# Kernel tuning notes

Measured on AMD Instinct MI355X. Metric: run time of the kernel, lower is better.

The kernel has to match this reference:

```python
import jax, jax.numpy as jnp
import numpy as np

B, D, H = 32, 512, 1024


def setup_inputs() -> dict:
    key = jax.random.key(0)
    ks = jax.random.split(key, 9)
    x = jax.random.normal(ks[0], (B, D), dtype=jnp.float32)
    h0 = 0.1 * jax.random.normal(ks[1], (B, H), dtype=jnp.float32)
    c0 = 0.1 * jax.random.normal(ks[2], (B, H), dtype=jnp.float32)
    # Hebbian trace lives in [-1, 1] (clipped each step)
    Hebb0 = jax.random.uniform(ks[3], (B, H, H), dtype=jnp.float32, minval=-0.5, maxval=0.5)
    weight_h = jax.random.normal(ks[4], (H, 4 * H), dtype=jnp.float32) / np.sqrt(H)
    weight_x = jax.random.normal(ks[5], (D, 4 * H), dtype=jnp.float32) / np.sqrt(D)
    # bias init: zeros, forget-gate slice set to 1 (T_max=None path)
    bias = jnp.zeros((4 * H,), dtype=jnp.float32).at[:H].set(1.0)
    # alpha init is constant 0.01; add tiny noise for non-degenerate testing
    alpha = 0.01 + 0.001 * jax.random.normal(ks[6], (H, H), dtype=jnp.float32)
    eta = jnp.array([0.01], dtype=jnp.float32)
    return {"x": x, "h0": h0, "c0": c0, "Hebb0": Hebb0,
            "weight_h": weight_h, "weight_x": weight_x, "bias": bias,
            "alpha": alpha, "eta": eta}


def reference(x, h0, c0, Hebb0, weight_h, weight_x, bias, alpha, eta):
    Hs = h0.shape[1]
    # gates = h0 @ (weight_h + cat[0,0,0, alpha*Hebb]) + x @ weight_x + bias
    # The plastic term only affects the last (cell-gate) chunk; compute it
    # without materializing the (B,H,4H) dynamic weight tensor.
    gates = h0 @ weight_h + x @ weight_x + bias[None, :]
    plastic = jnp.einsum('bi,ih,bih->bh', h0, alpha, Hebb0)  # (B, H)
    f_g, i_g, o_g, g_g = jnp.split(gates, 4, axis=1)
    g_g = g_g + plastic  # cell gate gets the fast-weight contribution
    tanh_g = jnp.tanh(g_g)
    c1 = jax.nn.sigmoid(f_g) * c0 + jax.nn.sigmoid(i_g) * tanh_g
    h1 = jax.nn.sigmoid(o_g) * jnp.tanh(c1)
    # Hebbian outer-product update with clip (neuromodulation=None path)
    Hebb1 = jnp.clip(Hebb0 + eta[0] * jnp.einsum('bh,bi->bhi', h0, tanh_g), -1.0, 1.0)
    return h1, c1, Hebb1
```

## Files before the change

kernel.cpp:

```cpp
#include <hip/hip_runtime.h>
#include <math.h>

#define B 32
#define D 512
#define H 1024
#define G4 4096
#define PCH 32
#define GCH 24

__global__ __launch_bounds__(256) void k_plastic(
    const float* __restrict__ h0, const float* __restrict__ alpha,
    const float* __restrict__ hebb, float* __restrict__ pp) {
  int blk = blockIdx.x;
  int b = blk >> 5;
  int c = blk & (PCH - 1);
  int h4 = threadIdx.x * 4;
  int i0 = c * (H / PCH);
  const float* hb = hebb + (size_t)b * H * H;
  float4 acc = make_float4(0.f, 0.f, 0.f, 0.f);
#pragma unroll 8
  for (int i = i0; i < i0 + (H / PCH); ++i) {
    float hv = h0[b * H + i];
    float4 a = *(const float4*)(alpha + (size_t)i * H + h4);
    float4 e = *(const float4*)(hb + (size_t)i * H + h4);
    acc.x += hv * a.x * e.x;
    acc.y += hv * a.y * e.y;
    acc.z += hv * a.z * e.z;
    acc.w += hv * a.w * e.w;
  }
  *(float4*)(pp + ((size_t)c * B + b) * H + h4) = acc;
}

__global__ __launch_bounds__(256) void k_gates(
    const float* __restrict__ h0, const float* __restrict__ x,
    const float* __restrict__ wh, const float* __restrict__ wx,
    float* __restrict__ gp) {
  int j = blockIdx.x * 256 + threadIdx.x;
  int c = blockIdx.y;
  float acc[B];
#pragma unroll
  for (int b = 0; b < B; ++b) acc[b] = 0.f;
  if (c < 16) {
    int i0 = c * 64;
#pragma unroll 8
    for (int i = i0; i < i0 + 64; ++i) {
      float w = wh[(size_t)i * G4 + j];
#pragma unroll
      for (int b = 0; b < B; ++b) acc[b] += h0[b * H + i] * w;
    }
  } else {
    int i0 = (c - 16) * 64;
#pragma unroll 8
    for (int i = i0; i < i0 + 64; ++i) {
      float w = wx[(size_t)i * G4 + j];
#pragma unroll
      for (int b = 0; b < B; ++b) acc[b] += x[b * D + i] * w;
    }
  }
#pragma unroll
  for (int b = 0; b < B; ++b) gp[((size_t)c * B + b) * G4 + j] = acc[b];
}

__global__ __launch_bounds__(256) void k_combine(
    const float* __restrict__ gp, const float* __restrict__ pp,
    const float* __restrict__ bias, const float* __restrict__ c0,
    float* __restrict__ out, float* __restrict__ tg_out) {
  int t = blockIdx.x * 256 + threadIdx.x;
  int b = t >> 10;
  int h = t & (H - 1);
  float sf = bias[h], si = bias[H + h], so = bias[2 * H + h], sg = bias[3 * H + h];
#pragma unroll
  for (int c = 0; c < GCH; ++c) {
    const float* g = gp + ((size_t)c * B + b) * G4;
    sf += g[h];
    si += g[H + h];
    so += g[2 * H + h];
    sg += g[3 * H + h];
  }
#pragma unroll
  for (int c = 0; c < PCH; ++c) sg += pp[((size_t)c * B + b) * H + h];
  float fg = 1.f / (1.f + expf(-sf));
  float ig = 1.f / (1.f + expf(-si));
  float og = 1.f / (1.f + expf(-so));
  float tgv = tanhf(sg);
  float c1 = fg * c0[t] + ig * tgv;
  float h1 = og * tanhf(c1);
  out[t] = h1;
  out[B * H + t] = c1;
  tg_out[t] = tgv;
}

__global__ __launch_bounds__(256) void k_hebb(
    const float* __restrict__ hebb, const float* __restrict__ h0,
    const float* __restrict__ tg, const float* __restrict__ eta,
    float* __restrict__ out) {
  int blk = blockIdx.x;
  int b = blk >> 7;
  int hg = blk & 127;
  int t4 = threadIdx.x * 4;
  float4 tv = *(const float4*)(tg + b * H + t4);
  float e = eta[0];
  size_t base = ((size_t)b * H + (size_t)hg * 8) * H + t4;
  const float* src = hebb + base;
  float* dst = out + base;
#pragma unroll
  for (int r = 0; r < 8; ++r) {
    float s = e * h0[b * H + hg * 8 + r];
    float4 v = *(const float4*)(src + (size_t)r * H);
    float4 rr;
    rr.x = fminf(fmaxf(v.x + s * tv.x, -1.f), 1.f);
    rr.y = fminf(fmaxf(v.y + s * tv.y, -1.f), 1.f);
    rr.z = fminf(fmaxf(v.z + s * tv.z, -1.f), 1.f);
    rr.w = fminf(fmaxf(v.w + s * tv.w, -1.f), 1.f);
    *(float4*)(dst + (size_t)r * H) = rr;
  }
}

extern "C" void kernel_launch(void* const* d_in, const int* in_sizes, int n_in,
                              void* d_out, int out_size, void* d_ws, size_t ws_size,
                              hipStream_t stream) {
  const float* x     = (const float*)d_in[0];
  const float* h0    = (const float*)d_in[1];
  const float* c0    = (const float*)d_in[2];
  const float* hebb  = (const float*)d_in[3];
  const float* wh    = (const float*)d_in[4];
  const float* wx    = (const float*)d_in[5];
  const float* bias  = (const float*)d_in[6];
  const float* alpha = (const float*)d_in[7];
  const float* eta   = (const float*)d_in[8];
  float* out = (float*)d_out;
  float* ws  = (float*)d_ws;

  float* pp = ws;
  float* gp = pp + (size_t)PCH * B * H;
  float* tg = gp + (size_t)GCH * B * G4;

  k_plastic<<<B * PCH, 256, 0, stream>>>(h0, alpha, hebb, pp);
  k_gates<<<dim3(16, GCH), 256, 0, stream>>>(h0, x, wh, wx, gp);
  k_combine<<<(B * H) / 256, 256, 0, stream>>>(gp, pp, bias, c0, out, tg);
  k_hebb<<<B * 128, 256, 0, stream>>>(hebb, h0, tg, eta, out + 2 * B * H);
}
```

Measured before the change: 326.0 us.

## Merge plastic and gate partial kernels into one heterogeneous launch

Folds the plastic-term reduction and the gate GEMV partials into a single kernel, with block index selecting the role, so both run concurrently instead of back-to-back. Split-K chunk counts are halved (fewer partials for the combine step to sum), and each gate block now covers 128 rows in two 16-batch halves to cut register pressure. The trade-off is longer per-block work and possible load imbalance between the two block types.

```diff
diff --git a/kernel.cpp b/kernel.cpp
--- a/kernel.cpp
+++ b/kernel.cpp
@@ -5,60 +5,61 @@
 #define D 512
 #define H 1024
 #define G4 4096
-#define PCH 32
-#define GCH 24
+#define PCH 16
+#define GCH 12
+#define NGATE (16 * GCH)
+#define NPLAST (B * PCH)
 
-__global__ __launch_bounds__(256) void k_plastic(
-    const float* __restrict__ h0, const float* __restrict__ alpha,
-    const float* __restrict__ hebb, float* __restrict__ pp) {
-  int blk = blockIdx.x;
-  int b = blk >> 5;
-  int c = blk & (PCH - 1);
-  int h4 = threadIdx.x * 4;
-  int i0 = c * (H / PCH);
-  const float* hb = hebb + (size_t)b * H * H;
-  float4 acc = make_float4(0.f, 0.f, 0.f, 0.f);
-#pragma unroll 8
-  for (int i = i0; i < i0 + (H / PCH); ++i) {
-    float hv = h0[b * H + i];
-    float4 a = *(const float4*)(alpha + (size_t)i * H + h4);
-    float4 e = *(const float4*)(hb + (size_t)i * H + h4);
-    acc.x += hv * a.x * e.x;
-    acc.y += hv * a.y * e.y;
-    acc.z += hv * a.z * e.z;
-    acc.w += hv * a.w * e.w;
-  }
-  *(float4*)(pp + ((size_t)c * B + b) * H + h4) = acc;
-}
-
-__global__ __launch_bounds__(256) void k_gates(
+__global__ __launch_bounds__(256) void k_partials(
     const float* __restrict__ h0, const float* __restrict__ x,
     const float* __restrict__ wh, const float* __restrict__ wx,
-    float* __restrict__ gp) {
-  int j = blockIdx.x * 256 + threadIdx.x;
-  int c = blockIdx.y;
-  float acc[B];
+    const float* __restrict__ alpha, const float* __restrict__ hebb,
+    float* __restrict__ gp, float* __restrict__ pp) {
+  int blk = blockIdx.x;
+  if (blk < NGATE) {
+    int c = blk % GCH;
+    int j = (blk / GCH) * 256 + threadIdx.x;
+    const float* Wp;
+    const float* in;
+    int i0, ld;
+    if (c < 8) { Wp = wh; in = h0; i0 = c * 128; ld = H; }
+    else       { Wp = wx; in = x;  i0 = (c - 8) * 128; ld = D; }
 #pragma unroll
-  for (int b = 0; b < B; ++b) acc[b] = 0.f;
-  if (c < 16) {
-    int i0 = c * 64;
-#pragma unroll 8
-    for (int i = i0; i < i0 + 64; ++i) {
-      float w = wh[(size_t)i * G4 + j];
+    for (int half = 0; half < 2; ++half) {
+      float acc[16];
 #pragma unroll
-      for (int b = 0; b < B; ++b) acc[b] += h0[b * H + i] * w;
+      for (int b = 0; b < 16; ++b) acc[b] = 0.f;
+      const float* inb = in + (size_t)(half * 16) * ld;
+#pragma unroll 2
+      for (int i = i0; i < i0 + 128; ++i) {
+        float w = Wp[(size_t)i * G4 + j];
+#pragma unroll
+        for (int b = 0; b < 16; ++b) acc[b] += inb[b * ld + i] * w;
+      }
+#pragma unroll
+      for (int b = 0; b < 16; ++b)
+        gp[((size_t)c * B + half * 16 + b) * G4 + j] = acc[b];
     }
   } else {
-    int i0 = (c - 16) * 64;
-#pragma unroll 8
-    for (int i = i0; i < i0 + 64; ++i) {
-      float w = wx[(size_t)i * G4 + j];
-#pragma unroll
-      for (int b = 0; b < B; ++b) acc[b] += x[b * D + i] * w;
+    int p = blk - NGATE;
+    int b = p >> 4;
+    int c = p & (PCH - 1);
+    int h4 = threadIdx.x * 4;
+    int i0 = c * (H / PCH);
+    const float* hb = hebb + (size_t)b * H * H;
+    float4 acc = make_float4(0.f, 0.f, 0.f, 0.f);
+#pragma unroll 4
+    for (int i = i0; i < i0 + (H / PCH); ++i) {
+      float hv = h0[b * H + i];
+      float4 a = *(const float4*)(alpha + (size_t)i * H + h4);
+      float4 e = *(const float4*)(hb + (size_t)i * H + h4);
+      acc.x += hv * a.x * e.x;
+      acc.y += hv * a.y * e.y;
+      acc.z += hv * a.z * e.z;
+      acc.w += hv * a.w * e.w;
     }
+    *(float4*)(pp + ((size_t)c * B + b) * H + h4) = acc;
   }
-#pragma unroll
-  for (int b = 0; b < B; ++b) gp[((size_t)c * B + b) * G4 + j] = acc[b];
 }
 
 __global__ __launch_bounds__(256) void k_combine(
@@ -135,8 +136,7 @@
   float* gp = pp + (size_t)PCH * B * H;
   float* tg = gp + (size_t)GCH * B * G4;
 
-  k_plastic<<<B * PCH, 256, 0, stream>>>(h0, alpha, hebb, pp);
-  k_gates<<<dim3(16, GCH), 256, 0, stream>>>(h0, x, wh, wx, gp);
+  k_partials<<<NGATE + NPLAST, 256, 0, stream>>>(h0, x, wh, wx, alpha, hebb, gp, pp);
   k_combine<<<(B * H) / 256, 256, 0, stream>>>(gp, pp, bias, c0, out, tg);
   k_hebb<<<B * 128, 256, 0, stream>>>(hebb, h0, tg, eta, out + 2 * B * H);
 }
```

After: 345.1 us. +5.8%, slower.

## Fuse LSTM phases into one cooperative kernel with grid syncs

Applied to the files above, without the earlier changes.

Merges the plastic-term, gate-GEMM, combine and Hebbian-update kernels into a single cooperative kernel of 1024 blocks that separates phases with grid-wide syncs. The plastic and gate partial work now run in the same phase so the blocks overlap, and the gate split is doubled to 48 chunks. The Hebbian output uses nontemporal stores. This is meant to remove launch gaps and improve load balance. The risks are grid sync cost, the occupancy limit of 4 blocks per CU, extra partial-sum traffic in combine, and a fallback to three separate launches if the cooperative launch fails.

```diff
diff --git a/kernel.cpp b/kernel.cpp
--- a/kernel.cpp
+++ b/kernel.cpp
@@ -1,75 +1,82 @@
 #include <hip/hip_runtime.h>
+#include <hip/hip_cooperative_groups.h>
 #include <math.h>
+
+namespace cg = cooperative_groups;
 
 #define B 32
 #define D 512
 #define H 1024
 #define G4 4096
 #define PCH 32
-#define GCH 24
+#define GCH 48
+#define NBLK 1024
 
-__global__ __launch_bounds__(256) void k_plastic(
-    const float* __restrict__ h0, const float* __restrict__ alpha,
-    const float* __restrict__ hebb, float* __restrict__ pp) {
-  int blk = blockIdx.x;
-  int b = blk >> 5;
-  int c = blk & (PCH - 1);
-  int h4 = threadIdx.x * 4;
-  int i0 = c * (H / PCH);
-  const float* hb = hebb + (size_t)b * H * H;
-  float4 acc = make_float4(0.f, 0.f, 0.f, 0.f);
+typedef float f4v __attribute__((ext_vector_type(4)));
+
+__device__ __forceinline__ void phase_partials(
+    int blk, int tid,
+    const float* __restrict__ x, const float* __restrict__ h0,
+    const float* __restrict__ wh, const float* __restrict__ wx,
+    const float* __restrict__ alpha, const float* __restrict__ hebb,
+    float* __restrict__ gp, float* __restrict__ pp) {
+  {
+    int b = blk >> 5;
+    int c = blk & (PCH - 1);
+    int h4 = tid * 4;
+    int i0 = c * (H / PCH);
+    const float* hb = hebb + (size_t)b * H * H;
+    float4 acc = make_float4(0.f, 0.f, 0.f, 0.f);
 #pragma unroll 8
-  for (int i = i0; i < i0 + (H / PCH); ++i) {
-    float hv = h0[b * H + i];
-    float4 a = *(const float4*)(alpha + (size_t)i * H + h4);
-    float4 e = *(const float4*)(hb + (size_t)i * H + h4);
-    acc.x += hv * a.x * e.x;
-    acc.y += hv * a.y * e.y;
-    acc.z += hv * a.z * e.z;
-    acc.w += hv * a.w * e.w;
+    for (int i = i0; i < i0 + (H / PCH); ++i) {
+      float hv = h0[b * H + i];
+      float4 a = *(const float4*)(alpha + (size_t)i * H + h4);
+      float4 e = *(const float4*)(hb + (size_t)i * H + h4);
+      acc.x += hv * a.x * e.x;
+      acc.y += hv * a.y * e.y;
+      acc.z += hv * a.z * e.z;
+      acc.w += hv * a.w * e.w;
+    }
+    *(float4*)(pp + ((size_t)c * B + b) * H + h4) = acc;
   }
-  *(float4*)(pp + ((size_t)c * B + b) * H + h4) = acc;
+  if (blk < 16 * GCH) {
+    int c = blk % GCH;
+    int j = (blk / GCH) * 256 + tid;
+    float acc[B];
+#pragma unroll
+    for (int b2 = 0; b2 < B; ++b2) acc[b2] = 0.f;
+    if (c < 32) {
+      int i0 = c * 32;
+#pragma unroll 8
+      for (int i = i0; i < i0 + 32; ++i) {
+        float w = wh[(size_t)i * G4 + j];
+#pragma unroll
+        for (int b2 = 0; b2 < B; ++b2) acc[b2] += h0[b2 * H + i] * w;
+      }
+    } else {
+      int i0 = (c - 32) * 32;
+#pragma unroll 8
+      for (int i = i0; i < i0 + 32; ++i) {
+        float w = wx[(size_t)i * G4 + j];
+#pragma unroll
+        for (int b2 = 0; b2 < B; ++b2) acc[b2] += x[b2 * D + i] * w;
+      }
+    }
+#pragma unroll
+    for (int b2 = 0; b2 < B; ++b2) gp[((size_t)c * B + b2) * G4 + j] = acc[b2];
+  }
 }
 
-__global__ __launch_bounds__(256) void k_gates(
-    const float* __restrict__ h0, const float* __restrict__ x,
-    const float* __restrict__ wh, const float* __restrict__ wx,
-    float* __restrict__ gp) {
-  int j = blockIdx.x * 256 + threadIdx.x;
-  int c = blockIdx.y;
-  float acc[B];
-#pragma unroll
-  for (int b = 0; b < B; ++b) acc[b] = 0.f;
-  if (c < 16) {
-    int i0 = c * 64;
-#pragma unroll 8
-    for (int i = i0; i < i0 + 64; ++i) {
-      float w = wh[(size_t)i * G4 + j];
-#pragma unroll
-      for (int b = 0; b < B; ++b) acc[b] += h0[b * H + i] * w;
-    }
-  } else {
-    int i0 = (c - 16) * 64;
-#pragma unroll 8
-    for (int i = i0; i < i0 + 64; ++i) {
-      float w = wx[(size_t)i * G4 + j];
-#pragma unroll
-      for (int b = 0; b < B; ++b) acc[b] += x[b * D + i] * w;
-    }
-  }
-#pragma unroll
-  for (int b = 0; b < B; ++b) gp[((size_t)c * B + b) * G4 + j] = acc[b];
-}
-
-__global__ __launch_bounds__(256) void k_combine(
+__device__ __forceinline__ void phase_combine(
+    int blk, int tid,
     const float* __restrict__ gp, const float* __restrict__ pp,
     const float* __restrict__ bias, const float* __restrict__ c0,
-    float* __restrict__ out, float* __restrict__ tg_out) {
-  int t = blockIdx.x * 256 + threadIdx.x;
+    float* __restrict__ out, float* __restrict__ tg) {
+  int t = blk * 256 + tid;
   int b = t >> 10;
   int h = t & (H - 1);
   float sf = bias[h], si = bias[H + h], so = bias[2 * H + h], sg = bias[3 * H + h];
-#pragma unroll
+#pragma unroll 8
   for (int c = 0; c < GCH; ++c) {
     const float* g = gp + ((size_t)c * B + b) * G4;
     sf += g[h];
@@ -77,7 +84,7 @@
     so += g[2 * H + h];
     sg += g[3 * H + h];
   }
-#pragma unroll
+#pragma unroll 8
   for (int c = 0; c < PCH; ++c) sg += pp[((size_t)c * B + b) * H + h];
   float fg = 1.f / (1.f + expf(-sf));
   float ig = 1.f / (1.f + expf(-si));
@@ -87,33 +94,74 @@
   float h1 = og * tanhf(c1);
   out[t] = h1;
   out[B * H + t] = c1;
-  tg_out[t] = tgv;
+  tg[t] = tgv;
 }
 
-__global__ __launch_bounds__(256) void k_hebb(
+__device__ __forceinline__ void phase_hebb(
+    int blk, int tid,
     const float* __restrict__ hebb, const float* __restrict__ h0,
     const float* __restrict__ tg, const float* __restrict__ eta,
-    float* __restrict__ out) {
+    float* __restrict__ hout) {
+  float e = eta[0];
+  int t4 = tid * 4;
+#pragma unroll
+  for (int k = 0; k < 4; ++k) {
+    int unit = blk * 4 + k;
+    int b = unit >> 7;
+    int hg = unit & 127;
+    float4 tv = *(const float4*)(tg + b * H + t4);
+    size_t base = ((size_t)b * H + (size_t)hg * 8) * H + t4;
+    const float* src = hebb + base;
+    float* dst = hout + base;
+#pragma unroll
+    for (int r = 0; r < 8; ++r) {
+      float s = e * h0[b * H + hg * 8 + r];
+      float4 v = *(const float4*)(src + (size_t)r * H);
+      f4v rr;
+      rr.x = fminf(fmaxf(v.x + s * tv.x, -1.f), 1.f);
+      rr.y = fminf(fmaxf(v.y + s * tv.y, -1.f), 1.f);
+      rr.z = fminf(fmaxf(v.z + s * tv.z, -1.f), 1.f);
+      rr.w = fminf(fmaxf(v.w + s * tv.w, -1.f), 1.f);
+      __builtin_nontemporal_store(rr, (f4v*)(dst + (size_t)r * H));
+    }
+  }
+}
+
+__global__ __launch_bounds__(256, 4) void k_coop(
+    const float* __restrict__ x, const float* __restrict__ h0,
+    const float* __restrict__ c0, const float* __restrict__ hebb,
+    const float* __restrict__ wh, const float* __restrict__ wx,
+    const float* __restrict__ bias, const float* __restrict__ alpha,
+    const float* __restrict__ eta,
+    float* __restrict__ out, float* __restrict__ hout,
+    float* __restrict__ pp, float* __restrict__ gp, float* __restrict__ tg) {
   int blk = blockIdx.x;
-  int b = blk >> 7;
-  int hg = blk & 127;
-  int t4 = threadIdx.x * 4;
-  float4 tv = *(const float4*)(tg + b * H + t4);
-  float e = eta[0];
-  size_t base = ((size_t)b * H + (size_t)hg * 8) * H + t4;
-  const float* src = hebb + base;
-  float* dst = out + base;
-#pragma unroll
-  for (int r = 0; r < 8; ++r) {
-    float s = e * h0[b * H + hg * 8 + r];
-    float4 v = *(const float4*)(src + (size_t)r * H);
-    float4 rr;
-    rr.x = fminf(fmaxf(v.x + s * tv.x, -1.f), 1.f);
-    rr.y = fminf(fmaxf(v.y + s * tv.y, -1.f), 1.f);
-    rr.z = fminf(fmaxf(v.z + s * tv.z, -1.f), 1.f);
-    rr.w = fminf(fmaxf(v.w + s * tv.w, -1.f), 1.f);
-    *(float4*)(dst + (size_t)r * H) = rr;
-  }
+  int tid = threadIdx.x;
+  phase_partials(blk, tid, x, h0, wh, wx, alpha, hebb, gp, pp);
+  cg::this_grid().sync();
+  if (blk < (B * H) / 256) phase_combine(blk, tid, gp, pp, bias, c0, out, tg);
+  cg::this_grid().sync();
+  phase_hebb(blk, tid, hebb, h0, tg, eta, hout);
+}
+
+__global__ __launch_bounds__(256, 4) void k_p1(
+    const float* __restrict__ x, const float* __restrict__ h0,
+    const float* __restrict__ wh, const float* __restrict__ wx,
+    const float* __restrict__ alpha, const float* __restrict__ hebb,
+    float* __restrict__ gp, float* __restrict__ pp) {
+  phase_partials(blockIdx.x, threadIdx.x, x, h0, wh, wx, alpha, hebb, gp, pp);
+}
+__global__ __launch_bounds__(256) void k_p2(
+    const float* __restrict__ gp, const float* __restrict__ pp,
+    const float* __restrict__ bias, const float* __restrict__ c0,
+    float* __restrict__ out, float* __restrict__ tg) {
+  phase_combine(blockIdx.x, threadIdx.x, gp, pp, bias, c0, out, tg);
+}
+__global__ __launch_bounds__(256, 4) void k_p3(
+    const float* __restrict__ hebb, const float* __restrict__ h0,
+    const float* __restrict__ tg, const float* __restrict__ eta,
+    float* __restrict__ hout) {
+  phase_hebb(blockIdx.x, threadIdx.x, hebb, h0, tg, eta, hout);
 }
 
 extern "C" void kernel_launch(void* const* d_in, const int* in_sizes, int n_in,
@@ -128,15 +176,23 @@
   const float* bias  = (const float*)d_in[6];
   const float* alpha = (const float*)d_in[7];
   const float* eta   = (const float*)d_in[8];
-  float* out = (float*)d_out;
-  float* ws  = (float*)d_ws;
+  float* out  = (float*)d_out;
+  float* hout = out + 2 * B * H;
+  float* ws   = (float*)d_ws;
 
   float* pp = ws;
   float* gp = pp + (size_t)PCH * B * H;
   float* tg = gp + (size_t)GCH * B * G4;
 
-  k_plastic<<<B * PCH, 256, 0, stream>>>(h0, alpha, hebb, pp);
-  k_gates<<<dim3(16, GCH), 256, 0, stream>>>(h0, x, wh, wx, gp);
-  k_combine<<<(B * H) / 256, 256, 0, stream>>>(gp, pp, bias, c0, out, tg);
-  k_hebb<<<B * 128, 256, 0, stream>>>(hebb, h0, tg, eta, out + 2 * B * H);
+  void* args[] = {(void*)&x, (void*)&h0, (void*)&c0, (void*)&hebb,
+                  (void*)&wh, (void*)&wx, (void*)&bias, (void*)&alpha,
+                  (void*)&eta, (void*)&out, (void*)&hout,
+                  (void*)&pp, (void*)&gp, (void*)&tg};
+  hipError_t err = hipLaunchCooperativeKernel(
+      (const void*)k_coop, dim3(NBLK), dim3(256), args, 0, stream);
+  if (err != hipSuccess) {
+    k_p1<<<NBLK, 256, 0, stream>>>(x, h0, wh, wx, alpha, hebb, gp, pp);
+    k_p2<<<(B * H) / 256, 256, 0, stream>>>(gp, pp, bias, c0, out, tg);
+    k_p3<<<NBLK, 256, 0, stream>>>(hebb, h0, tg, eta, hout);
+  }
 }
```

New measurement: 550.0 us. 1.69x slower.
